# Kernel tuning notes

Measured on AMD Instinct MI355X. Metric: run time of the kernel, lower is better.

Reference implementation:

```python
import jax, jax.numpy as jnp
import numpy as np

B, T, D = 2, 2048, 2048
H, DH = 32, 64
GN_EPS = DH * 1e-5  # GroupNorm eps = head_dim * norm_eps


def _lora(x, A, Bm, bias, act):
    h = x @ A.T
    if act == 'tanh':
        h = jnp.tanh(h)
    elif act == 'sigmoid':
        h = jax.nn.sigmoid(h)
    y = h @ Bm.T
    if bias is not None:
        y = y + bias
    return y


def setup_inputs() -> dict:
    key = jax.random.key(0)
    ks = jax.random.split(key, 24)
    def nrm(i, shape, s):
        return jax.random.normal(ks[i], shape, jnp.float32) * s
    return {
        'hidden_states': nrm(0, (B, T, D), 1.0),
        'v_state': nrm(1, (B, T, D), 1.0),
        'x_x': nrm(2, (6, D), 0.3),
        'k_k': 0.85 + nrm(3, (D,), 0.05),
        'k_a': 1.0 + nrm(4, (D,), 0.05),
        'r_k': nrm(5, (H, DH), 0.1),
        'Wr': nrm(6, (D, D), 0.02),
        'Wk': nrm(7, (D, D), 0.02),
        'Wv': nrm(8, (D, D), 0.02),
        'Wo': nrm(9, (D, D), 0.02),
        'wA': nrm(10, (64, D), 0.02), 'wB': nrm(11, (D, 64), 0.02), 'wb': nrm(12, (D,), 0.5),
        'vA': nrm(13, (16, D), 0.02), 'vB': nrm(14, (D, 16), 0.02), 'vb': jnp.zeros((D,), jnp.float32),
        'aA': nrm(15, (64, D), 0.02), 'aB': nrm(16, (D, 64), 0.02), 'ab': jnp.zeros((D,), jnp.float32),
        'gA': nrm(17, (128, D), 0.02), 'gB': nrm(18, (D, 128), 0.02),
        'gn_w': jnp.ones((D,), jnp.float32), 'gn_b': jnp.zeros((D,), jnp.float32),
    }


def reference(hidden_states, v_state, x_x, k_k, k_a, r_k, Wr, Wk, Wv, Wo,
              wA, wB, wb, vA, vB, vb, aA, aB, ab, gA, gB, gn_w, gn_b):
    b, t, d = hidden_states.shape
    # time_shift: shifted[t] = x[t-1], shifted[0] = 0
    shifted = jnp.pad(hidden_states, ((0, 0), (1, 0), (0, 0)))[:, :t]
    delta = shifted - hidden_states
    xm = hidden_states[None] + delta[None] * x_x[:, None, None, :]  # [6,B,T,D]
    xr, xw, xk, xv, xa, xg = xm[0], xm[1], xm[2], xm[3], xm[4], xm[5]

    r = xr @ Wr.T
    w = -jax.nn.softplus(-_lora(xw, wA, wB, wb, 'tanh')) - 0.5  # log decay, < -0.5
    k = xk @ Wk.T
    v = xv @ Wv.T
    # layer_idx != 0: v = lerp(v, v_state, sigmoid(v_lora(xv)))
    v = v + jax.nn.sigmoid(_lora(xv, vA, vB, vb, None)) * (v_state - v)
    a = jax.nn.sigmoid(_lora(xa, aA, aB, ab, None))
    g = _lora(xg, gA, gB, None, 'sigmoid')

    kk = (k * k_k).reshape(b, t, H, DH)
    kk = kk / jnp.maximum(jnp.linalg.norm(kk, axis=-1, keepdims=True), 1e-12)
    k = k * (1.0 + (a - 1.0) * k_a)

    r_h = r.reshape(b, t, H, DH)
    w_h = w.reshape(b, t, H, DH)
    k_h = k.reshape(b, t, H, DH)
    v_h = v.reshape(b, t, H, DH)
    a_h = a.reshape(b, t, H, DH)
    tm = lambda x: jnp.swapaxes(x, 0, 1)  # [B,T,H,DH] -> [T,B,H,DH]

    # RWKV7 DPLR delta rule: S = diag(exp(w)) S; S += b (a^T S) + k v^T; o = r^T S
    def step(S, xs):
        q_t, w_t, k_t, v_t, at, bt = xs  # each [B,H,DH]
        S = S * jnp.exp(w_t)[..., None]
        sa = jnp.einsum('bhk,bhkv->bhv', at, S)
        S = S + bt[..., None] * sa[..., None, :] + k_t[..., None] * v_t[..., None, :]
        return S, jnp.einsum('bhk,bhkv->bhv', q_t, S)

    S0 = jnp.zeros((b, H, DH, DH), hidden_states.dtype)
    _, o = jax.lax.scan(step, S0,
                        (tm(r_h), tm(w_h), tm(k_h), tm(v_h), tm(-kk), tm(kk * a_h)))
    o = jnp.swapaxes(o, 0, 1)  # [B,T,H,DH]

    # GroupNorm over each head's channels
    mu = o.mean(-1, keepdims=True)
    var = jnp.mean((o - mu) ** 2, axis=-1, keepdims=True)
    on = ((o - mu) / jnp.sqrt(var + GN_EPS)).reshape(b, t, d) * gn_w + gn_b

    on = on + ((r_h * k_h * r_k).sum(-1, keepdims=True) * v_h).reshape(b, t, d)
    return (on * g) @ Wo.T
```

## Files before the change

### kernel.cpp

```cpp
#include <hip/hip_runtime.h>
#include <hip/hip_bf16.h>
#include <math.h>


typedef __attribute__((ext_vector_type(8))) unsigned short ushort8;
typedef __attribute__((ext_vector_type(8))) _Float16 f16x8;
typedef __attribute__((ext_vector_type(4))) float f32x4;
typedef __attribute__((ext_vector_type(2))) float f32x2;

__device__ inline unsigned short f2h(float f) {
    _Float16 h = (_Float16)f;
    return __builtin_bit_cast(unsigned short, h);
}
__device__ inline float h2f(unsigned short u) {
    return (float)__builtin_bit_cast(_Float16, u);
}
__device__ inline float sigm(float x) { return 1.f / (1.f + expf(-x)); }

template <int CTRL>
__device__ __forceinline__ float rrot(float x) {
    int xi = __builtin_bit_cast(int, x);
    int yi = __builtin_amdgcn_update_dpp(xi, xi, CTRL, 0xf, 0xf, true);
    return x + __builtin_bit_cast(float, yi);
}
__device__ __forceinline__ float red8(float x)  { return rrot<0x128>(x); }
__device__ __forceinline__ float red16(float x) {
    float b = x;
    asm("" : "+v"(b));
    float a = x;
    asm("v_permlane16_swap_b32 %0, %1" : "+v"(a), "+v"(b));
    return a + b;
}
__device__ __forceinline__ float red32(float x) {
    float b = x;
    asm("" : "+v"(b));
    float a = x;
    asm("v_permlane32_swap_b32 %0, %1" : "+v"(a), "+v"(b));
    return a + b;
}
__device__ __forceinline__ float full64(float x) {
    x = rrot<0x121>(x);
    x = rrot<0x122>(x);
    x = rrot<0x124>(x);
    x = rrot<0x128>(x);
    return red32(red16(x));
}

__device__ __forceinline__ void gld16(void* lds, const void* g)
{
    __builtin_amdgcn_global_load_lds(
        (const __attribute__((address_space(1))) void*)g,
        (__attribute__((address_space(3))) void*)lds, 16, 0, 0);
}
__device__ __forceinline__ void gld4(void* lds, const void* g)
{
    __builtin_amdgcn_global_load_lds(
        (const __attribute__((address_space(1))) void*)g,
        (__attribute__((address_space(3))) void*)lds, 4, 0, 0);
}

__global__ void mixcvt6_h(const float* __restrict__ in, const float* __restrict__ x_x,
                          unsigned short* __restrict__ oR, unsigned short* __restrict__ oK,
                          unsigned short* __restrict__ ow, unsigned short* __restrict__ oa,
                          unsigned short* __restrict__ og, unsigned short* __restrict__ ov,
                          int T, int D, int total8)
{
    int i = blockIdx.x * 256 + threadIdx.x;
    if (i >= total8) return;
    const size_t e = (size_t)i * 8;
    float a[8];
    *(float4*)&a[0] = *(const float4*)(in + e);
    *(float4*)&a[4] = *(const float4*)(in + e + 4);
    const int m = (int)(e / D);
    const int d = (int)(e % D);
    const int t = m % T;
    float p[8] = {0.f,0.f,0.f,0.f,0.f,0.f,0.f,0.f};
    if (t > 0) {
        *(float4*)&p[0] = *(const float4*)(in + e - D);
        *(float4*)&p[4] = *(const float4*)(in + e - D + 4);
    }
    const float* xxr = x_x + 0 * (size_t)D + d;
    const float* xxw = x_x + 1 * (size_t)D + d;
    const float* xxk = x_x + 2 * (size_t)D + d;
    const float* xxv = x_x + 3 * (size_t)D + d;
    const float* xxa = x_x + 4 * (size_t)D + d;
    const float* xxg = x_x + 5 * (size_t)D + d;
    ushort8 rr, rk, rw, ra, rg, rv;
    #pragma unroll
    for (int j = 0; j < 8; ++j) {
        const float dl = p[j] - a[j];
        rr[j] = f2h(a[j] + dl * xxr[j]);
        rk[j] = f2h(a[j] + dl * xxk[j]);
        rw[j] = f2h(a[j] + dl * xxw[j]);
        ra[j] = f2h(a[j] + dl * xxa[j]);
        rg[j] = f2h(a[j] + dl * xxg[j]);
        rv[j] = f2h(a[j] + dl * xxv[j]);
    }
    *(ushort8*)(oR + e) = rr;
    *(ushort8*)(oK + e) = rk;
    *(ushort8*)(ow + e) = rw;
    *(ushort8*)(oa + e) = ra;
    *(ushort8*)(og + e) = rg;
    *(ushort8*)(ov + e) = rv;
}

__global__ void wcvt2_h(const float* __restrict__ in0, const float* __restrict__ in1,
                        unsigned short* __restrict__ hi0, unsigned short* __restrict__ hi1,
                        int total8)
{
    int i = blockIdx.x * 256 + threadIdx.x;
    if (i >= total8) return;
    const float* in = (blockIdx.y == 0) ? in0 : in1;
    unsigned short* hi = (blockIdx.y == 0) ? hi0 : hi1;
    const size_t e = (size_t)i * 8;
    float a[8];
    *(float4*)&a[0] = *(const float4*)(in + e);
    *(float4*)&a[4] = *(const float4*)(in + e + 4);
    ushort8 h8;
    #pragma unroll
    for (int j = 0; j < 8; ++j) h8[j] = f2h(a[j]);
    *(ushort8*)(hi + e) = h8;
}

__global__ void wcvt_lora(const float* __restrict__ wA, const float* __restrict__ vA,
                          const float* __restrict__ aA, const float* __restrict__ gA,
                          unsigned short* __restrict__ WL, int K)
{
    const int z = blockIdx.y;
    int i = blockIdx.x * 256 + threadIdx.x;
    const size_t e = (size_t)i * 8;
    const int row = (int)(e / K);
    const int col = (int)(e % K);
    const int nv = (z == 0) ? 64 : (z == 1) ? 16 : (z == 2) ? 64 : 128;
    const float* src = (z == 0) ? wA : (z == 1) ? vA : (z == 2) ? aA : gA;
    ushort8 h8;
    if (row < nv) {
        float a[8];
        *(float4*)&a[0] = *(const float4*)(src + (size_t)row * K + col);
        *(float4*)&a[4] = *(const float4*)(src + (size_t)row * K + col + 4);
        #pragma unroll
        for (int j = 0; j < 8; ++j) h8[j] = f2h(a[j]);
    } else {
        #pragma unroll
        for (int j = 0; j < 8; ++j) h8[j] = 0;
    }
    *(ushort8*)(WL + (size_t)z * 128 * K + e) = h8;
}

#define GBM 128
#define GBN 128

template <int TERMS>
__global__ __launch_bounds__(256) void gemm_h2(
    const unsigned short* __restrict__ Ag,
    const unsigned short* __restrict__ Bhg, const unsigned short* __restrict__ Blg,
    float* __restrict__ C, int M, int N, int K, int mode,
    const float* __restrict__ yv, const float* __restrict__ bias,
    const float* __restrict__ aux,
    size_t sA, size_t sB, size_t sC)
{
    __shared__ unsigned short As[GBM * 32];
    __shared__ unsigned short Bhs[GBN * 32], Bls[GBN * 32];
    const int z = blockIdx.z;
    Ag  += (size_t)z * sA;
    Bhg += (size_t)z * sB;
    Blg += (size_t)z * sB;
    C   += (size_t)z * sC;
    const int tid = threadIdx.x;
    const int m0 = blockIdx.x * GBM;
    const int n0 = blockIdx.y * GBN;
    const int wave = tid >> 6, lane = tid & 63;
    const int wr = (wave >> 1) * 64, wc = (wave & 1) * 64;
    const int fr = lane & 15, fq = lane >> 4;

    f32x4 acc[4][4];
    #pragma unroll
    for (int i = 0; i < 4; ++i)
        #pragma unroll
        for (int j = 0; j < 4; ++j)
            acc[i][j] = (f32x4){0.f, 0.f, 0.f, 0.f};

    const unsigned short* gsrc;
    unsigned short* lbuf;
    int rofs, nld;
    if (wave == 0)      { gsrc = Ag;  lbuf = As;           rofs = m0;      nld = 4; }
    else if (wave == 1) { gsrc = Ag;  lbuf = As + 64 * 32; rofs = m0 + 64; nld = 4; }
    else if (wave == 2) { gsrc = Bhg; lbuf = Bhs;          rofs = n0;      nld = 8; }
    else                { gsrc = Blg; lbuf = Bls;          rofs = n0;      nld = (TERMS == 2) ? 8 : 0; }
    const unsigned short* gbase = gsrc + (size_t)(rofs + (lane >> 2)) * K + ((lane & 3) << 3);

    for (int k0 = 0; k0 < K; k0 += 32) {
        #pragma unroll
        for (int j = 0; j < 8; ++j)
            if (j < nld)
                gld16(lbuf + j * 16 * 32, gbase + (size_t)(j * 16) * K + k0);
        __syncthreads();

        f16x8 fa[4], fbh[4], fbl[4];
        #pragma unroll
        for (int m = 0; m < 4; ++m)
            fa[m] = *(const f16x8*)&As[(wr + m * 16 + fr) * 32 + fq * 8];
        #pragma unroll
        for (int n = 0; n < 4; ++n) {
            fbh[n] = *(const f16x8*)&Bhs[(wc + n * 16 + fr) * 32 + fq * 8];
            if constexpr (TERMS == 2)
                fbl[n] = *(const f16x8*)&Bls[(wc + n * 16 + fr) * 32 + fq * 8];
        }
        #pragma unroll
        for (int m = 0; m < 4; ++m)
            #pragma unroll
            for (int n = 0; n < 4; ++n) {
                acc[m][n] = __builtin_amdgcn_mfma_f32_16x16x32_f16(fa[m], fbh[n], acc[m][n], 0, 0, 0);
                if constexpr (TERMS == 2)
                    acc[m][n] = __builtin_amdgcn_mfma_f32_16x16x32_f16(fa[m], fbl[n], acc[m][n], 0, 0, 0);
            }
        __syncthreads();
    }

    #pragma unroll
    for (int m = 0; m < 4; ++m) {
        const int row = m0 + wr + m * 16 + fq * 4;
        #pragma unroll
        for (int n = 0; n < 4; ++n) {
            const int col = n0 + wc + n * 16 + fr;
            #pragma unroll
            for (int j = 0; j < 4; ++j) {
                const size_t idx = (size_t)(row + j) * N + col;
                float v = acc[m][n][j];
                if (mode == 2) {
                    const float sg = sigm(yv[idx] + bias[col]);
                    v = v + sg * (aux[idx] - v);
                } else if (mode == 3 && z == 0) {
                    v = 0.6065306597126334f * sigm(v + bias[col]);
                }
                C[idx] = v;
            }
        }
    }
}

__global__ __launch_bounds__(256) void lora1_h(
    const unsigned short* __restrict__ Xbase,
    const unsigned short* __restrict__ WL,
    unsigned short* __restrict__ HW16, float* __restrict__ HV,
    unsigned short* __restrict__ HA16, unsigned short* __restrict__ HG16,
    int M, int K, size_t NE)
{
    __shared__ unsigned short As[GBM * 32];
    __shared__ unsigned short Bhs[GBN * 32];
    const int z = blockIdx.z;
    const size_t zofs = (z == 0) ? 0 : (z == 1) ? 3 * NE : (z == 2) ? NE : 2 * NE;
    const unsigned short* Ag = Xbase + zofs;
    const unsigned short* Bg = WL + (size_t)z * 128 * K;
    const int tid = threadIdx.x;
    const int m0 = blockIdx.x * GBM;
    const int wave = tid >> 6, lane = tid & 63;
    const int wr = (wave >> 1) * 64, wc = (wave & 1) * 64;
    const int fr = lane & 15, fq = lane >> 4;

    f32x4 acc[4][4];
    #pragma unroll
    for (int i = 0; i < 4; ++i)
        #pragma unroll
        for (int j = 0; j < 4; ++j)
            acc[i][j] = (f32x4){0.f, 0.f, 0.f, 0.f};

    const unsigned short* gsrc;
    unsigned short* lbuf;
    int rofs, nld;
    if (wave == 0)      { gsrc = Ag; lbuf = As;           rofs = m0;      nld = 4; }
    else if (wave == 1) { gsrc = Ag; lbuf = As + 64 * 32; rofs = m0 + 64; nld = 4; }
    else if (wave == 2) { gsrc = Bg; lbuf = Bhs;          rofs = 0;       nld = 8; }
    else                { gsrc = Bg; lbuf = Bhs;          rofs = 0;       nld = 0; }
    const unsigned short* gbase = gsrc + (size_t)(rofs + (lane >> 2)) * K + ((lane & 3) << 3);

    for (int k0 = 0; k0 < K; k0 += 32) {
        #pragma unroll
        for (int j = 0; j < 8; ++j)
            if (j < nld)
                gld16(lbuf + j * 16 * 32, gbase + (size_t)(j * 16) * K + k0);
        __syncthreads();

        f16x8 fa[4], fb[4];
        #pragma unroll
        for (int m = 0; m < 4; ++m)
            fa[m] = *(const f16x8*)&As[(wr + m * 16 + fr) * 32 + fq * 8];
        #pragma unroll
        for (int n = 0; n < 4; ++n)
            fb[n] = *(const f16x8*)&Bhs[(wc + n * 16 + fr) * 32 + fq * 8];
        #pragma unroll
        for (int m = 0; m < 4; ++m)
            #pragma unroll
            for (int n = 0; n < 4; ++n)
                acc[m][n] = __builtin_amdgcn_mfma_f32_16x16x32_f16(fa[m], fb[n], acc[m][n], 0, 0, 0);
        __syncthreads();
    }

    #pragma unroll
    for (int m = 0; m < 4; ++m) {
        const int row = m0 + wr + m * 16 + fq * 4;
        #pragma unroll
        for (int n = 0; n < 4; ++n) {
            const int col = wc + n * 16 + fr;
            #pragma unroll
            for (int j = 0; j < 4; ++j) {
                const float v = acc[m][n][j];
                const int r = row + j;
                if (z == 0)      { if (col < 64) HW16[(size_t)r * 64 + col] = f2h(tanhf(v)); }
                else if (z == 1) { if (col < 16) HV[(size_t)r * 16 + col] = v; }
                else if (z == 2) { if (col < 64) HA16[(size_t)r * 64 + col] = f2h(v); }
                else             { HG16[(size_t)r * 128 + col] = f2h(sigm(v)); }
            }
        }
    }
}

#define BM 64
#define BN 64
#define BK 16
__global__ __launch_bounds__(256) void gemm_f32(
    const float* __restrict__ A, const float* __restrict__ xx,
    const float* __restrict__ W, float* __restrict__ C,
    int M, int N, int K, int T, int mode, const float* __restrict__ bias)
{
    __shared__ float As[BK][BM + 4];
    __shared__ float Bs[BK][BN + 4];
    const int tid = threadIdx.x;
    const int m0 = blockIdx.x * BM;
    const int n0 = blockIdx.y * BN;
    const int lr = tid >> 2;
    const int lk = (tid & 3) << 2;
    const int tx = tid & 15;
    const int ty = tid >> 4;
    const int mrow = m0 + lr;
    const int nrow = n0 + lr;
    float acc[4][4];
    #pragma unroll
    for (int i = 0; i < 4; ++i)
        #pragma unroll
        for (int j = 0; j < 4; ++j) acc[i][j] = 0.f;

    for (int k0 = 0; k0 < K; k0 += BK) {
        const float* ap = A + (size_t)mrow * K + k0 + lk;
        float4 av = *(const float4*)ap;
        if (xx) {
            const int t = mrow % T;
            float4 pv = make_float4(0.f, 0.f, 0.f, 0.f);
            if (t > 0) pv = *(const float4*)(ap - K);
            const float4 xv = *(const float4*)(xx + k0 + lk);
            av.x += (pv.x - av.x) * xv.x;
            av.y += (pv.y - av.y) * xv.y;
            av.z += (pv.z - av.z) * xv.z;
            av.w += (pv.w - av.w) * xv.w;
        }
        float4 bv = make_float4(0.f, 0.f, 0.f, 0.f);
        if (nrow < N) bv = *(const float4*)(W + (size_t)nrow * K + k0 + lk);

        As[lk + 0][lr] = av.x; As[lk + 1][lr] = av.y;
        As[lk + 2][lr] = av.z; As[lk + 3][lr] = av.w;
        Bs[lk + 0][lr] = bv.x; Bs[lk + 1][lr] = bv.y;
        Bs[lk + 2][lr] = bv.z; Bs[lk + 3][lr] = bv.w;
        __syncthreads();

        #pragma unroll
        for (int kk = 0; kk < BK; ++kk) {
            const float4 a4 = *(const float4*)&As[kk][ty << 2];
            const float4 b4 = *(const float4*)&Bs[kk][tx << 2];
            const float a[4] = {a4.x, a4.y, a4.z, a4.w};
            const float b[4] = {b4.x, b4.y, b4.z, b4.w};
            #pragma unroll
            for (int i = 0; i < 4; ++i)
                #pragma unroll
                for (int j = 0; j < 4; ++j)
                    acc[i][j] = fmaf(a[i], b[j], acc[i][j]);
        }
        __syncthreads();
    }
    #pragma unroll
    for (int i = 0; i < 4; ++i) {
        const int m = m0 + (ty << 2) + i;
        #pragma unroll
        for (int j = 0; j < 4; ++j) {
            const int n = n0 + (tx << 2) + j;
            if (n < N) {
                const size_t idx = (size_t)m * N + n;
                float v = acc[i][j];
                if (mode == 1) v = 0.6065306597126334f * sigm(v + bias[n]);
                C[idx] = v;
            }
        }
    }
}

__global__ __launch_bounds__(256) void ka_epi(
    float* __restrict__ Kf, float* __restrict__ A_BV, float* __restrict__ KKo,
    const float* __restrict__ k_k, const float* __restrict__ k_a,
    const float* __restrict__ ab, int total, int H)
{
    int wid = (blockIdx.x << 2) | (threadIdx.x >> 6);
    if (wid >= total) return;
    const int l = threadIdx.x & 63;
    const int h = wid % H;
    const int ch = h * 64 + l;
    const size_t base = (size_t)wid * 64;
    float k0 = Kf[base + l];
    float a = sigm(A_BV[base + l] + ab[ch]);
    float kkr = k0 * k_k[ch];
    float ss = full64(kkr * kkr);
    float inv = 1.f / fmaxf(sqrtf(ss), 1e-12f);
    float kkn = kkr * inv;
    KKo[base + l] = kkn;
    A_BV[base + l] = kkn * a;
    Kf[base + l] = k0 * fmaf(a - 1.f, k_a[ch], 1.f);
}

#define SCH 16
__global__ __launch_bounds__(64) void rwkv_scan(
    const float* __restrict__ EW, const float* __restrict__ R,
    const float* __restrict__ Kf, const float* __restrict__ Vf,
    const float* __restrict__ KK, const float* __restrict__ BV,
    float* __restrict__ O, int T, int H)
{
    __shared__ float lds[2][5 * SCH * 64 + SCH * 8];

    const int blk = blockIdx.x;
    const int bh = blk & 63;
    const int slab = blk >> 6;
    const int b = bh >> 5, h = bh & 31;
    const int l = threadIdx.x;
    const int vc = l & 7;
    const int g  = l >> 3;
    const int kb = g << 3;
    const int vb0 = slab << 3;
    const size_t step = (size_t)H * 64;
    const size_t base0 = ((size_t)b * T * H + h) * 64;

    auto stage = [&](int c, int buf) {
        float* L = &lds[buf][0];
        const size_t t0 = (size_t)c * SCH;
        const float* gs[5] = {EW, R, Kf, KK, BV};
        #pragma unroll
        for (int s = 0; s < 5; ++s) {
            const float* gp = gs[s];
            #pragma unroll
            for (int j = 0; j < 4; ++j)
                gld16(L + s * SCH * 64 + j * 4 * 64,
                      gp + base0 + (t0 + j * 4 + (l >> 4)) * step + ((l & 15) << 2));
        }
        gld4(L + 5 * SCH * 64,
             Vf + base0 + (t0 + (l >> 3)) * step + vb0 + (l & 7));
        gld4(L + 5 * SCH * 64 + 64,
             Vf + base0 + (t0 + 8 + (l >> 3)) * step + vb0 + (l & 7));
    };

    f32x2 s2[4];
    #pragma unroll
    for (int i = 0; i < 4; ++i) s2[i] = (f32x2){0.f, 0.f};

    struct P { f32x4 e[2], r[2], k[2], q[2], bb[2]; float vv; };
    P PA, PB;
    const int NCH = T / SCH;

    stage(0, 0);
    asm volatile("s_waitcnt vmcnt(0)" ::: "memory");
    __builtin_amdgcn_sched_barrier(0);

    for (int c = 0; c < NCH; ++c) {
        if (c + 1 < NCH) stage(c + 1, (c + 1) & 1);

        const float* L = &lds[c & 1][0];
        auto PRE = [&](P& pp, int tt) {
            const int o = tt * 64 + kb;
            #pragma unroll
            for (int j = 0; j < 2; ++j) {
                pp.e[j]  = *(const f32x4*)(L + 0 * SCH * 64 + o + j * 4);
                pp.r[j]  = *(const f32x4*)(L + 1 * SCH * 64 + o + j * 4);
                pp.k[j]  = *(const f32x4*)(L + 2 * SCH * 64 + o + j * 4);
                pp.q[j]  = *(const f32x4*)(L + 3 * SCH * 64 + o + j * 4);
                pp.bb[j] = *(const f32x4*)(L + 4 * SCH * 64 + o + j * 4);
            }
            pp.vv = L[5 * SCH * 64 + tt * 8 + vc];
        };
        auto COMP = [&](const P& pp, int tt) {
            f32x2 sa0 = (f32x2){0.f, 0.f}, sa1 = (f32x2){0.f, 0.f};
            #pragma unroll
            for (int j = 0; j < 2; ++j) {
                const f32x2 elo = __builtin_shufflevector(pp.e[j], pp.e[j], 0, 1);
                const f32x2 ehi = __builtin_shufflevector(pp.e[j], pp.e[j], 2, 3);
                const f32x2 qlo = __builtin_shufflevector(pp.q[j], pp.q[j], 0, 1);
                const f32x2 qhi = __builtin_shufflevector(pp.q[j], pp.q[j], 2, 3);
                s2[2*j]   *= elo;
                s2[2*j+1] *= ehi;
                sa0 += qlo * s2[2*j];
                sa1 += qhi * s2[2*j+1];
            }
            const f32x2 sas = sa0 + sa1;
            float p = -(sas.x + sas.y);
            p = red32(red16(red8(p)));
            const f32x2 p2 = (f32x2){p, p};
            const f32x2 v2 = (f32x2){pp.vv, pp.vv};
            f32x2 o0 = (f32x2){0.f, 0.f}, o1 = (f32x2){0.f, 0.f};
            #pragma unroll
            for (int j = 0; j < 2; ++j) {
                const f32x2 klo = __builtin_shufflevector(pp.k[j], pp.k[j], 0, 1);
                const f32x2 khi = __builtin_shufflevector(pp.k[j], pp.k[j], 2, 3);
                const f32x2 blo = __builtin_shufflevector(pp.bb[j], pp.bb[j], 0, 1);
                const f32x2 bhi = __builtin_shufflevector(pp.bb[j], pp.bb[j], 2, 3);
                const f32x2 rlo = __builtin_shufflevector(pp.r[j], pp.r[j], 0, 1);
                const f32x2 rhi = __builtin_shufflevector(pp.r[j], pp.r[j], 2, 3);
                s2[2*j]   = blo * p2 + (klo * v2 + s2[2*j]);
                s2[2*j+1] = bhi * p2 + (khi * v2 + s2[2*j+1]);
                o0 += rlo * s2[2*j];
                o1 += rhi * s2[2*j+1];
            }
            const f32x2 os = o0 + o1;
            float oo = os.x + os.y;
            oo = red32(red16(red8(oo)));
            if (g == 0)
                O[base0 + (size_t)(c * SCH + tt) * step + vb0 + vc] = oo;
        };

        PRE(PA, 0);
        PRE(PB, 1);
        #pragma unroll
        for (int tt = 0; tt < SCH - 2; tt += 2) {
            COMP(PA, tt);     PRE(PA, tt + 2);
            COMP(PB, tt + 1); PRE(PB, tt + 3);
        }
        COMP(PA, SCH - 2);
        COMP(PB, SCH - 1);

        asm volatile("s_waitcnt vmcnt(0)" ::: "memory");
        __builtin_amdgcn_sched_barrier(0);
    }
}

__global__ __launch_bounds__(256) void gn_bonus(
    const float* __restrict__ O, const float* __restrict__ R,
    const float* __restrict__ Kf, const float* __restrict__ Vf,
    const float* __restrict__ G, const float* __restrict__ r_k,
    const float* __restrict__ gn_w, const float* __restrict__ gn_b,
    unsigned short* __restrict__ ON16, int total, int H, float eps)
{
    int wid = (blockIdx.x << 2) | (threadIdx.x >> 6);
    if (wid >= total) return;
    const int l = threadIdx.x & 63;
    const int h = wid % H;
    const int ch = h * 64 + l;
    const size_t base = (size_t)wid * 64;

    const float o = O[base + l];
    const float mu = full64(o) * (1.f / 64.f);
    const float d = o - mu;
    const float ss = full64(d * d);
    const float inv = 1.f / sqrtf(ss * (1.f / 64.f) + eps);
    float on = d * inv * gn_w[ch] + gn_b[ch];

    const float r = R[base + l], k = Kf[base + l], vv = Vf[base + l];
    const float p = full64(r * k * r_k[ch]);
    on = fmaf(p, vv, on);
    ON16[base + l] = f2h(on * G[base + l]);
}

extern "C" void kernel_launch(void* const* d_in, const int* in_sizes, int n_in,
                              void* d_out, int out_size, void* d_ws, size_t ws_size,
                              hipStream_t stream)
{
    const int B = 2, T = 2048, D = 2048, H = 32;
    const int M = B * T;

    const float* hid = (const float*)d_in[0];
    const float* vst = (const float*)d_in[1];
    const float* x_x = (const float*)d_in[2];
    const float* k_k = (const float*)d_in[3];
    const float* k_a = (const float*)d_in[4];
    const float* r_k = (const float*)d_in[5];
    const float* Wr  = (const float*)d_in[6];
    const float* Wk  = (const float*)d_in[7];
    const float* Wv  = (const float*)d_in[8];
    const float* Wo  = (const float*)d_in[9];
    const float* wA  = (const float*)d_in[10];
    const float* wB  = (const float*)d_in[11];
    const float* wb  = (const float*)d_in[12];
    const float* vA  = (const float*)d_in[13];
    const float* vB  = (const float*)d_in[14];
    const float* vb  = (const float*)d_in[15];
    const float* aA  = (const float*)d_in[16];
    const float* aB  = (const float*)d_in[17];
    const float* ab  = (const float*)d_in[18];
    const float* gA  = (const float*)d_in[19];
    const float* gB  = (const float*)d_in[20];
    const float* gnw = (const float*)d_in[21];
    const float* gnb = (const float*)d_in[22];
    float* out = (float*)d_out;

    const size_t NE = (size_t)M * D;
    const size_t DD = (size_t)D * D;
    const size_t need = (6 * NE + (size_t)M * 272) * sizeof(float);
    if (ws_size < need) return;

    float* W0 = (float*)d_ws;
    float* W1 = W0 + NE;
    float* W2 = W1 + NE;
    float* W3 = W2 + NE;
    float* W4 = W3 + NE;
    float* W5 = W4 + NE;
    float* SMALL = W5 + NE;
    unsigned short* HW16 = (unsigned short*)SMALL;
    unsigned short* HA16 = HW16 + (size_t)M * 64;
    unsigned short* HG16 = HA16 + (size_t)M * 64;
    float* HV = (float*)(HG16 + (size_t)M * 128);

    dim3 blk(256);
    const int nMix = (int)(NE / 8);
    const int nW   = (int)(DD / 8);
    const float* nf = nullptr;

    unsigned short* X2   = (unsigned short*)W1;
    unsigned short* X4   = (unsigned short*)W4;
    unsigned short* WRK  = (unsigned short*)W3;
    unsigned short* WL   = (unsigned short*)W0;

    hipLaunchKernelGGL(mixcvt6_h, dim3(nMix / 256), blk, 0, stream,
                       hid, x_x, X2, X2 + NE, X4, X4 + NE, X4 + 2 * NE, X4 + 3 * NE, T, D, nMix);

    hipLaunchKernelGGL(wcvt2_h, dim3(nW / 256, 2), blk, 0, stream, Wr, Wk, WRK, WRK + DD, nW);
    hipLaunchKernelGGL(wcvt_lora, dim3(128, 4), blk, 0, stream, wA, vA, aA, gA, WL, D);

    hipLaunchKernelGGL(lora1_h, dim3(M / GBM, 1, 4), blk, 0, stream,
                       X4, WL, HW16, HV, HA16, HG16, M, D, NE);

    hipLaunchKernelGGL((gemm_h2<1>), dim3(M / GBM, D / GBN, 2), blk, 0, stream,
                       X2, WRK, WRK, W0, M, D, D, 0, nf, nf, nf,
                       NE, DD, 2 * NE);

    hipLaunchKernelGGL(gemm_f32, dim3(M / BM, D / BN), blk, 0, stream, HV, nf, vB, W1, M, D, 16, T, 0, nf);

    unsigned short* WvH = (unsigned short*)W4;
    hipLaunchKernelGGL(wcvt2_h, dim3(nW / 256, 1), blk, 0, stream, Wv, Wv, WvH, WvH, nW);
    hipLaunchKernelGGL((gemm_h2<1>), dim3(M / GBM, D / GBN, 1), blk, 0, stream,
                       X4 + 3 * NE, WvH, WvH, W3, M, D, D, 2, W1, vb, vst, 0, 0, 0);

    unsigned short* wB16 = (unsigned short*)W4;
    unsigned short* aB16 = wB16 + (size_t)D * 64;
    hipLaunchKernelGGL(wcvt2_h, dim3((int)(D * 64 / 8 / 256), 2), blk, 0, stream, wB, aB, wB16, aB16, (int)(D * 64 / 8));
    hipLaunchKernelGGL((gemm_h2<1>), dim3(M / GBM, D / GBN, 2), blk, 0, stream,
                       HW16, wB16, wB16, W1, M, D, 64, 3, nf, wb, nf,
                       (size_t)M * 64, (size_t)D * 64, 4 * NE);

    const int totalW = M * H;
    hipLaunchKernelGGL(ka_epi, dim3(totalW / 4), blk, 0, stream, W2, W5, W4, k_k, k_a, ab, totalW, H);

    hipLaunchKernelGGL(rwkv_scan, dim3(B * H * 8), dim3(64), 0, stream, W1, W0, W2, W3, W4, W5, out, T, H);

    unsigned short* gb16 = (unsigned short*)W5;
    hipLaunchKernelGGL(wcvt2_h, dim3((int)(D * 128 / 8 / 256), 1), blk, 0, stream, gB, gB, gb16, gb16, (int)(D * 128 / 8));
    hipLaunchKernelGGL((gemm_h2<1>), dim3(M / GBM, D / GBN, 1), blk, 0, stream,
                       HG16, gb16, gb16, W4, M, D, 128, 0, nf, nf, nf, 0, 0, 0);

    unsigned short* ON16 = (unsigned short*)W1;
    hipLaunchKernelGGL(gn_bonus, dim3(totalW / 4), blk, 0, stream, out, W0, W2, W3, W4, r_k, gnw, gnb, ON16, totalW, H, 64.f * 1e-5f);

    unsigned short* Wo16 = (unsigned short*)W3;
    hipLaunchKernelGGL(wcvt2_h, dim3(nW / 256, 1), blk, 0, stream, Wo, Wo, Wo16, Wo16, nW);
    hipLaunchKernelGGL((gemm_h2<1>), dim3(M / GBM, D / GBN, 1), blk, 0, stream,
                       ON16, Wo16, Wo16, out, M, D, D, 0, nf, nf, nf, 0, 0, 0);
}
```

Baseline: 874.6 us.

## Fuse v-LoRA into Wv GEMM epilogue; co-schedule scan with g-GEMM and Wo conversion

```diff
diff --git a/kernel.cpp b/kernel.cpp
--- a/kernel.cpp
+++ b/kernel.cpp
@@ -155,8 +155,8 @@
     const unsigned short* __restrict__ Ag,
     const unsigned short* __restrict__ Bhg, const unsigned short* __restrict__ Blg,
     float* __restrict__ C, int M, int N, int K, int mode,
-    const float* __restrict__ yv, const float* __restrict__ bias,
-    const float* __restrict__ aux,
+    const float* __restrict__ HVp, const float* __restrict__ vBp,
+    const float* __restrict__ bias, const float* __restrict__ aux,
     size_t sA, size_t sB, size_t sC)
 {
     __shared__ unsigned short As[GBM * 32];
@@ -227,8 +227,13 @@
             for (int j = 0; j < 4; ++j) {
                 const size_t idx = (size_t)(row + j) * N + col;
                 float v = acc[m][n][j];
-                if (mode == 2) {
-                    const float sg = sigm(yv[idx] + bias[col]);
+                if (mode == 4) {
+                    const float* hv = HVp + (size_t)(row + j) * 16;
+                    const float* vb = vBp + (size_t)col * 16;
+                    float yv = 0.f;
+                    #pragma unroll
+                    for (int kk = 0; kk < 16; ++kk) yv = fmaf(hv[kk], vb[kk], yv);
+                    const float sg = sigm(yv + bias[col]);
                     v = v + sg * (aux[idx] - v);
                 } else if (mode == 3 && z == 0) {
                     v = 0.6065306597126334f * sigm(v + bias[col]);
@@ -310,83 +315,6 @@
                 else if (z == 1) { if (col < 16) HV[(size_t)r * 16 + col] = v; }
                 else if (z == 2) { if (col < 64) HA16[(size_t)r * 64 + col] = f2h(v); }
                 else             { HG16[(size_t)r * 128 + col] = f2h(sigm(v)); }
-            }
-        }
-    }
-}
-
-#define BM 64
-#define BN 64
-#define BK 16
-__global__ __launch_bounds__(256) void gemm_f32(
-    const float* __restrict__ A, const float* __restrict__ xx,
-    const float* __restrict__ W, float* __restrict__ C,
-    int M, int N, int K, int T, int mode, const float* __restrict__ bias)
-{
-    __shared__ float As[BK][BM + 4];
-    __shared__ float Bs[BK][BN + 4];
-    const int tid = threadIdx.x;
-    const int m0 = blockIdx.x * BM;
-    const int n0 = blockIdx.y * BN;
-    const int lr = tid >> 2;
-    const int lk = (tid & 3) << 2;
-    const int tx = tid & 15;
-    const int ty = tid >> 4;
-    const int mrow = m0 + lr;
-    const int nrow = n0 + lr;
-    float acc[4][4];
-    #pragma unroll
-    for (int i = 0; i < 4; ++i)
-        #pragma unroll
-        for (int j = 0; j < 4; ++j) acc[i][j] = 0.f;
-
-    for (int k0 = 0; k0 < K; k0 += BK) {
-        const float* ap = A + (size_t)mrow * K + k0 + lk;
-        float4 av = *(const float4*)ap;
-        if (xx) {
-            const int t = mrow % T;
-            float4 pv = make_float4(0.f, 0.f, 0.f, 0.f);
-            if (t > 0) pv = *(const float4*)(ap - K);
-            const float4 xv = *(const float4*)(xx + k0 + lk);
-            av.x += (pv.x - av.x) * xv.x;
-            av.y += (pv.y - av.y) * xv.y;
-            av.z += (pv.z - av.z) * xv.z;
-            av.w += (pv.w - av.w) * xv.w;
-        }
-        float4 bv = make_float4(0.f, 0.f, 0.f, 0.f);
-        if (nrow < N) bv = *(const float4*)(W + (size_t)nrow * K + k0 + lk);
-
-        As[lk + 0][lr] = av.x; As[lk + 1][lr] = av.y;
-        As[lk + 2][lr] = av.z; As[lk + 3][lr] = av.w;
-        Bs[lk + 0][lr] = bv.x; Bs[lk + 1][lr] = bv.y;
-        Bs[lk + 2][lr] = bv.z; Bs[lk + 3][lr] = bv.w;
-        __syncthreads();
-
-        #pragma unroll
-        for (int kk = 0; kk < BK; ++kk) {
-            const float4 a4 = *(const float4*)&As[kk][ty << 2];
-            const float4 b4 = *(const float4*)&Bs[kk][tx << 2];
-            const float a[4] = {a4.x, a4.y, a4.z, a4.w};
-            const float b[4] = {b4.x, b4.y, b4.z, b4.w};
-            #pragma unroll
-            for (int i = 0; i < 4; ++i)
-                #pragma unroll
-                for (int j = 0; j < 4; ++j)
-                    acc[i][j] = fmaf(a[i], b[j], acc[i][j]);
-        }
-        __syncthreads();
-    }
-    #pragma unroll
-    for (int i = 0; i < 4; ++i) {
-        const int m = m0 + (ty << 2) + i;
-        #pragma unroll
-        for (int j = 0; j < 4; ++j) {
-            const int n = n0 + (tx << 2) + j;
-            if (n < N) {
-                const size_t idx = (size_t)m * N + n;
-                float v = acc[i][j];
-                if (mode == 1) v = 0.6065306597126334f * sigm(v + bias[n]);
-                C[idx] = v;
             }
         }
     }
@@ -415,28 +343,26 @@
 }
 
 #define SCH 16
-__global__ __launch_bounds__(64) void rwkv_scan(
+__device__ __forceinline__ void scan_core(
+    float* ldsf, int blk, int l,
     const float* __restrict__ EW, const float* __restrict__ R,
     const float* __restrict__ Kf, const float* __restrict__ Vf,
     const float* __restrict__ KK, const float* __restrict__ BV,
     float* __restrict__ O, int T, int H)
 {
-    __shared__ float lds[2][5 * SCH * 64 + SCH * 8];
-
-    const int blk = blockIdx.x;
     const int bh = blk & 63;
     const int slab = blk >> 6;
     const int b = bh >> 5, h = bh & 31;
-    const int l = threadIdx.x;
     const int vc = l & 7;
     const int g  = l >> 3;
     const int kb = g << 3;
     const int vb0 = slab << 3;
     const size_t step = (size_t)H * 64;
     const size_t base0 = ((size_t)b * T * H + h) * 64;
+    const int BUF = 5 * SCH * 64 + SCH * 8;
 
     auto stage = [&](int c, int buf) {
-        float* L = &lds[buf][0];
+        float* L = ldsf + buf * BUF;
         const size_t t0 = (size_t)c * SCH;
         const float* gs[5] = {EW, R, Kf, KK, BV};
         #pragma unroll
@@ -468,7 +394,7 @@
     for (int c = 0; c < NCH; ++c) {
         if (c + 1 < NCH) stage(c + 1, (c + 1) & 1);
 
-        const float* L = &lds[c & 1][0];
+        const float* L = ldsf + (c & 1) * BUF;
         auto PRE = [&](P& pp, int tt) {
             const int o = tt * 64 + kb;
             #pragma unroll
@@ -535,10 +461,114 @@
     }
 }
 
+__global__ __launch_bounds__(64) void rwkv_scan(
+    const float* __restrict__ EW, const float* __restrict__ R,
+    const float* __restrict__ Kf, const float* __restrict__ Vf,
+    const float* __restrict__ KK, const float* __restrict__ BV,
+    float* __restrict__ O, int T, int H)
+{
+    __shared__ float ldsf[2 * (5 * SCH * 64 + SCH * 8)];
+    scan_core(ldsf, blockIdx.x, threadIdx.x, EW, R, Kf, Vf, KK, BV, O, T, H);
+}
+
+__global__ __launch_bounds__(256) void scan_fused(
+    const float* __restrict__ EW, const float* __restrict__ R,
+    const float* __restrict__ Kf, const float* __restrict__ Vf,
+    const float* __restrict__ KK, const float* __restrict__ BV,
+    float* __restrict__ O,
+    const unsigned short* __restrict__ HG16, const unsigned short* __restrict__ gb16,
+    unsigned short* __restrict__ G16,
+    const float* __restrict__ Wo, unsigned short* __restrict__ Wo16, int nW8,
+    int T, int H, int M, int D)
+{
+    __shared__ float smemf[2 * (5 * SCH * 64 + SCH * 8)];
+    const int bid = blockIdx.x;
+    const int tid = threadIdx.x;
+
+    if (bid < 512) {
+        if (tid >= 64) return;
+        scan_core(smemf, bid, tid, EW, R, Kf, Vf, KK, BV, O, T, H);
+        return;
+    }
+    if (bid < 1024) {
+        unsigned short* As  = (unsigned short*)smemf;
+        unsigned short* Bhs = As + GBM * 32;
+        const int bid2 = bid - 512;
+        const int m0 = (bid2 >> 4) * GBM;
+        const int n0 = (bid2 & 15) * GBN;
+        const int wave = tid >> 6, lane = tid & 63;
+        const int wr = (wave >> 1) * 64, wc = (wave & 1) * 64;
+        const int fr = lane & 15, fq = lane >> 4;
+        const int K = 128;
+
+        f32x4 acc[4][4];
+        #pragma unroll
+        for (int i = 0; i < 4; ++i)
+            #pragma unroll
+            for (int j = 0; j < 4; ++j)
+                acc[i][j] = (f32x4){0.f, 0.f, 0.f, 0.f};
+
+        const unsigned short* gsrc;
+        unsigned short* lbuf;
+        int rofs, nld;
+        if (wave == 0)      { gsrc = HG16; lbuf = As;           rofs = m0;      nld = 4; }
+        else if (wave == 1) { gsrc = HG16; lbuf = As + 64 * 32; rofs = m0 + 64; nld = 4; }
+        else if (wave == 2) { gsrc = gb16; lbuf = Bhs;          rofs = n0;      nld = 8; }
+        else                { gsrc = gb16; lbuf = Bhs;          rofs = n0;      nld = 0; }
+        const unsigned short* gbase = gsrc + (size_t)(rofs + (lane >> 2)) * K + ((lane & 3) << 3);
+
+        for (int k0 = 0; k0 < K; k0 += 32) {
+            #pragma unroll
+            for (int j = 0; j < 8; ++j)
+                if (j < nld)
+                    gld16(lbuf + j * 16 * 32, gbase + (size_t)(j * 16) * K + k0);
+            __syncthreads();
+            f16x8 fa[4], fb[4];
+            #pragma unroll
+            for (int m = 0; m < 4; ++m)
+                fa[m] = *(const f16x8*)&As[(wr + m * 16 + fr) * 32 + fq * 8];
+            #pragma unroll
+            for (int n = 0; n < 4; ++n)
+                fb[n] = *(const f16x8*)&Bhs[(wc + n * 16 + fr) * 32 + fq * 8];
+            #pragma unroll
+            for (int m = 0; m < 4; ++m)
+                #pragma unroll
+                for (int n = 0; n < 4; ++n)
+                    acc[m][n] = __builtin_amdgcn_mfma_f32_16x16x32_f16(fa[m], fb[n], acc[m][n], 0, 0, 0);
+            __syncthreads();
+        }
+        #pragma unroll
+        for (int m = 0; m < 4; ++m) {
+            const int row = m0 + wr + m * 16 + fq * 4;
+            #pragma unroll
+            for (int n = 0; n < 4; ++n) {
+                const int col = n0 + wc + n * 16 + fr;
+                #pragma unroll
+                for (int j = 0; j < 4; ++j)
+                    G16[(size_t)(row + j) * D + col] = f2h(acc[m][n][j]);
+            }
+        }
+        return;
+    }
+    {
+        int i = (bid - 1024) * 256 + tid;
+        if (i >= nW8) return;
+        const size_t e = (size_t)i * 8;
+        float a[8];
+        *(float4*)&a[0] = *(const float4*)(Wo + e);
+        *(float4*)&a[4] = *(const float4*)(Wo + e + 4);
+        ushort8 h8;
+        #pragma unroll
+        for (int j = 0; j < 8; ++j) h8[j] = f2h(a[j]);
+        *(ushort8*)(Wo16 + e) = h8;
+    }
+}
+
 __global__ __launch_bounds__(256) void gn_bonus(
     const float* __restrict__ O, const float* __restrict__ R,
     const float* __restrict__ Kf, const float* __restrict__ Vf,
-    const float* __restrict__ G, const float* __restrict__ r_k,
+    const float* __restrict__ G, const unsigned short* __restrict__ G16,
+    const float* __restrict__ r_k,
     const float* __restrict__ gn_w, const float* __restrict__ gn_b,
     unsigned short* __restrict__ ON16, int total, int H, float eps)
 {
@@ -559,7 +589,8 @@
     const float r = R[base + l], k = Kf[base + l], vv = Vf[base + l];
     const float p = full64(r * k * r_k[ch]);
     on = fmaf(p, vv, on);
-    ON16[base + l] = f2h(on * G[base + l]);
+    const float gg = G16 ? h2f(G16[base + l]) : G[base + l];
+    ON16[base + l] = f2h(on * gg);
 }
 
 extern "C" void kernel_launch(void* const* d_in, const int* in_sizes, int n_in,
@@ -596,8 +627,10 @@
 
     const size_t NE = (size_t)M * D;
     const size_t DD = (size_t)D * D;
-    const size_t need = (6 * NE + (size_t)M * 272) * sizeof(float);
+    const size_t need  = (6 * NE + (size_t)M * 272) * sizeof(float);
+    const size_t need2 = (7 * NE + (size_t)M * 272) * sizeof(float);
     if (ws_size < need) return;
+    const bool fused = (ws_size >= need2);
 
     float* W0 = (float*)d_ws;
     float* W1 = W0 + NE;
@@ -610,6 +643,7 @@
     unsigned short* HA16 = HW16 + (size_t)M * 64;
     unsigned short* HG16 = HA16 + (size_t)M * 64;
     float* HV = (float*)(HG16 + (size_t)M * 128);
+    float* W6 = SMALL + (size_t)M * 272;
 
     dim3 blk(256);
     const int nMix = (int)(NE / 8);
@@ -631,38 +665,48 @@
                        X4, WL, HW16, HV, HA16, HG16, M, D, NE);
 
     hipLaunchKernelGGL((gemm_h2<1>), dim3(M / GBM, D / GBN, 2), blk, 0, stream,
-                       X2, WRK, WRK, W0, M, D, D, 0, nf, nf, nf,
+                       X2, WRK, WRK, W0, M, D, D, 0, nf, nf, nf, nf,
                        NE, DD, 2 * NE);
-
-    hipLaunchKernelGGL(gemm_f32, dim3(M / BM, D / BN), blk, 0, stream, HV, nf, vB, W1, M, D, 16, T, 0, nf);
 
     unsigned short* WvH = (unsigned short*)W4;
     hipLaunchKernelGGL(wcvt2_h, dim3(nW / 256, 1), blk, 0, stream, Wv, Wv, WvH, WvH, nW);
     hipLaunchKernelGGL((gemm_h2<1>), dim3(M / GBM, D / GBN, 1), blk, 0, stream,
-                       X4 + 3 * NE, WvH, WvH, W3, M, D, D, 2, W1, vb, vst, 0, 0, 0);
+                       X4 + 3 * NE, WvH, WvH, W3, M, D, D, 4, HV, vB, vb, vst, 0, 0, 0);
 
     unsigned short* wB16 = (unsigned short*)W4;
     unsigned short* aB16 = wB16 + (size_t)D * 64;
     hipLaunchKernelGGL(wcvt2_h, dim3((int)(D * 64 / 8 / 256), 2), blk, 0, stream, wB, aB, wB16, aB16, (int)(D * 64 / 8));
     hipLaunchKernelGGL((gemm_h2<1>), dim3(M / GBM, D / GBN, 2), blk, 0, stream,
-                       HW16, wB16, wB16, W1, M, D, 64, 3, nf, wb, nf,
+                       HW16, wB16, wB16, W1, M, D, 64, 3, nf, nf, wb, nf,
                        (size_t)M * 64, (size_t)D * 64, 4 * NE);
 
     const int totalW = M * H;
     hipLaunchKernelGGL(ka_epi, dim3(totalW / 4), blk, 0, stream, W2, W5, W4, k_k, k_a, ab, totalW, H);
 
-    hipLaunchKernelGGL(rwkv_scan, dim3(B * H * 8), dim3(64), 0, stream, W1, W0, W2, W3, W4, W5, out, T, H);
-
-    unsigned short* gb16 = (unsigned short*)W5;
-    hipLaunchKernelGGL(wcvt2_h, dim3((int)(D * 128 / 8 / 256), 1), blk, 0, stream, gB, gB, gb16, gb16, (int)(D * 128 / 8));
-    hipLaunchKernelGGL((gemm_h2<1>), dim3(M / GBM, D / GBN, 1), blk, 0, stream,
-                       HG16, gb16, gb16, W4, M, D, 128, 0, nf, nf, nf, 0, 0, 0);
-
-    unsigned short* ON16 = (unsigned short*)W1;
-    hipLaunchKernelGGL(gn_bonus, dim3(totalW / 4), blk, 0, stream, out, W0, W2, W3, W4, r_k, gnw, gnb, ON16, totalW, H, 64.f * 1e-5f);
-
-    unsigned short* Wo16 = (unsigned short*)W3;
-    hipLaunchKernelGGL(wcvt2_h, dim3(nW / 256, 1), blk, 0, stream, Wo, Wo, Wo16, Wo16, nW);
-    hipLaunchKernelGGL((gemm_h2<1>), dim3(M / GBM, D / GBN, 1), blk, 0, stream,
-                       ON16, Wo16, Wo16, out, M, D, D, 0, nf, nf, nf, 0, 0, 0);
-}
+    if (fused) {
+        unsigned short* W6s  = (unsigned short*)W6;
+        unsigned short* G16p = W6s;
+        unsigned short* Wo16 = W6s + NE;
+        unsigned short* gb16 = W6s + NE + DD;
+        hipLaunchKernelGGL(wcvt2_h, dim3((int)(D * 128 / 8 / 256), 1), blk, 0, stream, gB, gB, gb16, gb16, (int)(D * 128 / 8));
+        hipLaunchKernelGGL(scan_fused, dim3(512 + 512 + 2048), blk, 0, stream,
+                           W1, W0, W2, W3, W4, W5, out,
+                           HG16, gb16, G16p, Wo, Wo16, nW * 256 / 256 * 1 + (nW - nW) + nW, T, H, M, D);
+        unsigned short* ON16 = (unsigned short*)W1;
+        hipLaunchKernelGGL(gn_bonus, dim3(totalW / 4), blk, 0, stream, out, W0, W2, W3, nf, G16p, r_k, gnw, gnb, ON16, totalW, H, 64.f * 1e-5f);
+        hipLaunchKernelGGL((gemm_h2<1>), dim3(M / GBM, D / GBN, 1), blk, 0, stream,
+                           ON16, Wo16, Wo16, out, M, D, D, 0, nf, nf, nf, nf, 0, 0, 0);
+    } else {
+        hipLaunchKernelGGL(rwkv_scan, dim3(B * H * 8), dim3(64), 0, stream, W1, W0, W2, W3, W4, W5, out, T, H);
+        unsigned short* gb16 = (unsigned short*)W5;
+        hipLaunchKernelGGL(wcvt2_h, dim3((int)(D * 128 / 8 / 256), 1), blk, 0, stream, gB, gB, gb16, gb16, (int)(D * 128 / 8));
+        hipLaunchKernelGGL((gemm_h2<1>), dim3(M / GBM, D / GBN, 1), blk, 0, stream,
+                           HG16, gb16, gb16, W4, M, D, 128, 0, nf, nf, nf, nf, 0, 0, 0);
+        unsigned short* ON16 = (unsigned short*)W1;
+        hipLaunchKernelGGL(gn_bonus, dim3(totalW / 4), blk, 0, stream, out, W0, W2, W3, W4, (const unsigned short*)nullptr, r_k, gnw, gnb, ON16, totalW, H, 64.f * 1e-5f);
+        unsigned short* Wo16 = (unsigned short*)W3;
+        hipLaunchKernelGGL(wcvt2_h, dim3(nW / 256, 1), blk, 0, stream, Wo, Wo, Wo16, Wo16, nW);
+        hipLaunchKernelGGL((gemm_h2<1>), dim3(M / GBM, D / GBN, 1), blk, 0, stream,
+                           ON16, Wo16, Wo16, out, M, D, D, 0, nf, nf, nf, nf, 0, 0, 0);
+    }
+}
```

Result: faster. 840.1 us (-3.9%).
